# Kernel tuning notes

Measured on AMD Instinct MI355X. Metric: run time of the kernel, lower is better.

The kernel has to match this reference:

```python
import jax, jax.numpy as jnp
import numpy as np

B, T, F, H, L = 16384, 24, 7, 8, 4
DENSE = [T * H, 1024, 2048, 4]


def setup_inputs() -> dict:
    key = jax.random.key(0)
    d = {"x": jax.random.normal(jax.random.fold_in(key, 0), (B, T, F), jnp.float32)}
    k = 1
    s = 1.0 / np.sqrt(H)  # torch LSTM init bound
    for l in range(L):
        in_dim = F if l == 0 else H
        for name, shape in [("Wih", (4 * H, in_dim)), ("Whh", (4 * H, H)), ("bih", (4 * H,)), ("bhh", (4 * H,))]:
            d[f"{name}{l}"] = jax.random.uniform(jax.random.fold_in(key, k), shape, jnp.float32, -s, s)
            k += 1
    for i in range(1, len(DENSE)):
        si = 1.0 / np.sqrt(DENSE[i - 1])
        d[f"Wd{i}"] = jax.random.uniform(jax.random.fold_in(key, k), (DENSE[i], DENSE[i - 1]), jnp.float32, -si, si)
        k += 1
        d[f"bd{i}"] = jax.random.uniform(jax.random.fold_in(key, k), (DENSE[i],), jnp.float32, -si, si)
        k += 1
    return d


def _lstm_layer(xs, Wih, Whh, b):
    # xs: [T, B, in] -> ys: [T, B, H]; torch gate order i,f,g,o
    Hn = Whh.shape[1]
    h0 = jnp.zeros((xs.shape[1], Hn), xs.dtype)

    def step(carry, xt):
        h, c = carry
        z = xt @ Wih.T + h @ Whh.T + b  # [B, 4H]
        i, f, g, o = jnp.split(z, 4, axis=-1)
        c = jax.nn.sigmoid(f) * c + jax.nn.sigmoid(i) * jnp.tanh(g)
        h = jax.nn.sigmoid(o) * jnp.tanh(c)
        return (h, c), h

    (_, _), ys = jax.lax.scan(step, (h0, h0), xs)
    return ys


def _forward(x, lstm_params, dense_params):
    xs = jnp.transpose(x, (1, 0, 2))  # [T, B, F]
    for (Wih, Whh, bih, bhh) in lstm_params:
        xs = _lstm_layer(xs, Wih, Whh, bih + bhh)
    out = jnp.transpose(xs, (1, 0, 2)).reshape(x.shape[0], T * H)  # [B, 192]
    (W1, b1), (W2, b2), (W3, b3) = dense_params
    out = jax.nn.relu(out @ W1.T + b1)
    out = jax.nn.relu(out @ W2.T + b2)
    return out @ W3.T + b3  # [B, num_classes]


def reference(x, Wih0, Whh0, bih0, bhh0, Wih1, Whh1, bih1, bhh1, Wih2, Whh2, bih2, bhh2, Wih3, Whh3, bih3, bhh3, Wd1, bd1, Wd2, bd2, Wd3, bd3):
    lstm_params = [(Wih0, Whh0, bih0, bhh0), (Wih1, Whh1, bih1, bhh1), (Wih2, Whh2, bih2, bhh2), (Wih3, Whh3, bih3, bhh3)]
    dense_params = [(Wd1, bd1), (Wd2, bd2), (Wd3, bd3)]
    return _forward(x, lstm_params, dense_params)
```

## Files before the change

kernel.cpp:

```cpp
#include <hip/hip_runtime.h>
#include <hip/hip_bf16.h>

typedef __attribute__((ext_vector_type(4))) float f32x4;
typedef __attribute__((ext_vector_type(16))) float f32x16;
typedef __attribute__((ext_vector_type(2))) float f32x2;
typedef __attribute__((ext_vector_type(8))) short bf16x8;

__device__ __forceinline__ ushort f2bf(float f) {
    union { float f; uint u; } v; v.f = f;
    uint u = v.u;
    return (ushort)((u + 0x7fffu + ((u >> 16) & 1u)) >> 16);
}
__device__ __forceinline__ float sigm(float x) {
    return __builtin_amdgcn_rcpf(1.0f + __builtin_amdgcn_exp2f(x * -1.442695040888963f));
}
__device__ __forceinline__ float tanh_(float x) {
    return 2.0f * __builtin_amdgcn_rcpf(1.0f + __builtin_amdgcn_exp2f(x * -2.885390081777927f)) - 1.0f;
}

typedef const __attribute__((address_space(1))) unsigned int ga_u32;
typedef __attribute__((address_space(3))) unsigned int lds_u32;
__device__ __forceinline__ void g2l16(const void* g, void* l) {
    __builtin_amdgcn_global_load_lds((ga_u32*)(unsigned long long)g,
                                     (lds_u32*)(unsigned int)(unsigned long long)l,
                                     16, 0, 0);
}

struct LstmW {
    const float* wih[4];
    const float* whh[4];
    const float* bih[4];
    const float* bhh[4];
};

__device__ __forceinline__ void gates8p(const f32x2 w01[8], const f32x2 w23[8],
                                        const float xv8[8], f32x2& a01, f32x2& a23) {
#pragma unroll
    for (int k = 0; k < 8; ++k) {
        f32x2 xv = {xv8[k], xv8[k]};
        a01 += w01[k] * xv;
        a23 += w23[k] * xv;
    }
}
__device__ __forceinline__ void cellup(f32x2 a01, f32x2 a23, float& h, float& c) {
    c = sigm(a01.y) * c + sigm(a01.x) * tanh_(a23.x);
    h = sigm(a23.y) * tanh_(c);
}
__device__ __forceinline__ void ld8(const float* p, float v[8]) {
    float4 a = *(const float4*)p;
    float4 b = *(const float4*)(p + 4);
    v[0] = a.x; v[1] = a.y; v[2] = a.z; v[3] = a.w;
    v[4] = b.x; v[5] = b.y; v[6] = b.z; v[7] = b.w;
}

__global__ __launch_bounds__(256) void pre_kernel(const float* __restrict__ x, LstmW p,
                                                  ushort* __restrict__ Y,
                                                  const float* __restrict__ W1,
                                                  const float* __restrict__ W2,
                                                  ushort* __restrict__ W1b,
                                                  ushort* __restrict__ W2b,
                                                  const float* __restrict__ b3,
                                                  float* __restrict__ out) {
    __shared__ float xs[32 * 168];
    __shared__ float hb[32 * 200];

    const int tid = threadIdx.x;
    if (blockIdx.x >= 512) {
        const int tg = (blockIdx.x - 512) * 256 + tid;
        if (tg < 16384) {
            float4 bv = {b3[0], b3[1], b3[2], b3[3]};
            ((float4*)out)[tg] = bv;
        }
#pragma unroll
        for (int s = 0; s < 4; ++s) {
            int i = tg + s * 143360;
            const float4* src; ushort4* dst; int off;
            if (i < 49152) { src = (const float4*)W1; dst = (ushort4*)W1b; off = i; }
            else { src = (const float4*)W2; dst = (ushort4*)W2b; off = i - 49152; }
            float4 v = src[off];
            ushort4 r; r.x = f2bf(v.x); r.y = f2bf(v.y); r.z = f2bf(v.z); r.w = f2bf(v.w);
            dst[off] = r;
        }
        return;
    }

    const int e0 = blockIdx.x * 32;
    {
        const float4* s = (const float4*)(x + (size_t)e0 * 168);
        float4* d = (float4*)xs;
        for (int i = tid; i < 1344; i += 256) d[i] = s[i];
    }
    __syncthreads();

    const int el = tid >> 3, j = tid & 7;
    float* hr = hb + el * 200;
    const float* xr = xs + el * 168;

    f32x2 wx01[8], wx23[8], wh01[8], wh23[8], b01, b23;

    {
        const float* Wih = p.wih[0];
        const float* Whh = p.whh[0];
#pragma unroll
        for (int k = 0; k < 7; ++k) {
            wx01[k] = {Wih[(0 + j) * 7 + k], Wih[(8 + j) * 7 + k]};
            wx23[k] = {Wih[(16 + j) * 7 + k], Wih[(24 + j) * 7 + k]};
        }
#pragma unroll
        for (int k = 0; k < 8; ++k) {
            wh01[k] = {Whh[(0 + j) * 8 + k], Whh[(8 + j) * 8 + k]};
            wh23[k] = {Whh[(16 + j) * 8 + k], Whh[(24 + j) * 8 + k]};
        }
        b01 = {p.bih[0][j] + p.bhh[0][j], p.bih[0][8 + j] + p.bhh[0][8 + j]};
        b23 = {p.bih[0][16 + j] + p.bhh[0][16 + j], p.bih[0][24 + j] + p.bhh[0][24 + j]};

        float h = 0.f, c = 0.f;
        {
            f32x2 a01 = b01, a23 = b23;
#pragma unroll
            for (int k = 0; k < 7; ++k) {
                f32x2 xv = {xr[k], xr[k]};
                a01 += wx01[k] * xv; a23 += wx23[k] * xv;
            }
            cellup(a01, a23, h, c);
            hr[j] = h;
        }
        for (int t = 1; t < 24; ++t) {
            f32x2 a01 = b01, a23 = b23;
#pragma unroll
            for (int k = 0; k < 7; ++k) {
                f32x2 xv = {xr[t * 7 + k], xr[t * 7 + k]};
                a01 += wx01[k] * xv; a23 += wx23[k] * xv;
            }
            float hp[8]; ld8(&hr[(t - 1) * 8], hp);
            gates8p(wh01, wh23, hp, a01, a23);
            cellup(a01, a23, h, c);
            hr[t * 8 + j] = h;
        }
    }

#pragma unroll
    for (int l = 1; l < 4; ++l) {
        const float* Wih = p.wih[l];
        const float* Whh = p.whh[l];
#pragma unroll
        for (int k = 0; k < 8; ++k) {
            wx01[k] = {Wih[(0 + j) * 8 + k], Wih[(8 + j) * 8 + k]};
            wx23[k] = {Wih[(16 + j) * 8 + k], Wih[(24 + j) * 8 + k]};
            wh01[k] = {Whh[(0 + j) * 8 + k], Whh[(8 + j) * 8 + k]};
            wh23[k] = {Whh[(16 + j) * 8 + k], Whh[(24 + j) * 8 + k]};
        }
        b01 = {p.bih[l][j] + p.bhh[l][j], p.bih[l][8 + j] + p.bhh[l][8 + j]};
        b23 = {p.bih[l][16 + j] + p.bhh[l][16 + j], p.bih[l][24 + j] + p.bhh[l][24 + j]};

        float h = 0.f, c = 0.f;
        {
            float xin[8]; ld8(&hr[0], xin);
            f32x2 a01 = b01, a23 = b23;
            gates8p(wx01, wx23, xin, a01, a23);
            cellup(a01, a23, h, c);
            hr[j] = h;
            if (l == 3) Y[((size_t)(e0 + el) * 24) * 8 + j] = f2bf(h);
        }
        for (int t = 1; t < 24; ++t) {
            float xin[8]; ld8(&hr[t * 8], xin);
            float hp[8];  ld8(&hr[(t - 1) * 8], hp);
            f32x2 a01 = b01, a23 = b23;
            gates8p(wx01, wx23, xin, a01, a23);
            gates8p(wh01, wh23, hp, a01, a23);
            cellup(a01, a23, h, c);
            hr[t * 8 + j] = h;
            if (l == 3) Y[((size_t)(e0 + el) * 24 + t) * 8 + j] = f2bf(h);
        }
    }
}

template <int KDIM>
__device__ __forceinline__ void gemm_body(const ushort* __restrict__ A,
                                          const ushort* __restrict__ W,
                                          const float* __restrict__ bias,
                                          ushort* __restrict__ Hout, int N) {
    __shared__ alignas(16) ushort smem[16384];
    ushort* As = smem;
    ushort* Ws = smem + 8192;

    const int tid = threadIdx.x;
    const int m0 = blockIdx.x * 128;
    const int n0 = blockIdx.y * 128;
    const int lane = tid & 63;
    const int wv = tid >> 6;
    const int wm = (wv & 1) * 64;
    const int wn = (wv >> 1) * 64;
    const int l31 = lane & 31;
    const int kh = lane >> 5;

    const int lrow = lane >> 3;
    const int lchunk = (lane & 7) ^ lrow;
    const ushort* Ag = A + (size_t)(m0 + wv * 32 + lrow) * KDIM + lchunk * 8;
    const ushort* Wg = W + (size_t)(n0 + wv * 32 + lrow) * KDIM + lchunk * 8;
    ushort* Ald = As + wv * 2048;
    ushort* Wld = Ws + wv * 2048;

    const int r7 = l31 & 7;
    const int arow0 = (wm + l31) * 64;
    const int brow0 = (wn + l31) * 64;

    f32x16 acc[2][2];
#pragma unroll
    for (int mi = 0; mi < 2; ++mi)
#pragma unroll
        for (int ni = 0; ni < 2; ++ni)
#pragma unroll
            for (int r = 0; r < 16; ++r) acc[mi][ni][r] = 0.f;

    for (int k0 = 0; k0 < KDIM; k0 += 64) {
#pragma unroll
        for (int c = 0; c < 4; ++c)
            g2l16(Ag + (size_t)c * 8 * KDIM + k0, Ald + c * 512);
#pragma unroll
        for (int c = 0; c < 4; ++c)
            g2l16(Wg + (size_t)c * 8 * KDIM + k0, Wld + c * 512);
        __syncthreads();

#pragma unroll
        for (int ks = 0; ks < 4; ++ks) {
            const int ck = ((ks * 2 + kh) ^ r7) * 8;
            bf16x8 afr[2], bfr[2];
#pragma unroll
            for (int mi = 0; mi < 2; ++mi)
                afr[mi] = *(const bf16x8*)&As[arow0 + mi * 2048 + ck];
#pragma unroll
            for (int ni = 0; ni < 2; ++ni)
                bfr[ni] = *(const bf16x8*)&Ws[brow0 + ni * 2048 + ck];
#pragma unroll
            for (int mi = 0; mi < 2; ++mi)
#pragma unroll
                for (int ni = 0; ni < 2; ++ni)
                    acc[mi][ni] = __builtin_amdgcn_mfma_f32_32x32x16_bf16(afr[mi], bfr[ni],
                                                                         acc[mi][ni], 0, 0, 0);
        }
        __syncthreads();
    }

#pragma unroll
    for (int ni = 0; ni < 2; ++ni) {
        const int col = n0 + wn + ni * 32 + l31;
        const float b = bias[col];
#pragma unroll
        for (int mi = 0; mi < 2; ++mi)
#pragma unroll
            for (int r = 0; r < 16; ++r) {
                const int row = m0 + wm + mi * 32 + (r & 3) + 8 * (r >> 2) + 4 * kh;
                Hout[(size_t)row * N + col] = f2bf(fmaxf(acc[mi][ni][r] + b, 0.f));
            }
    }
}

__global__ __launch_bounds__(256, 4) void gemm1_kernel(const ushort* __restrict__ A,
                                                       const ushort* __restrict__ W,
                                                       const float* __restrict__ bias,
                                                       ushort* __restrict__ Hout, int N) {
    gemm_body<192>(A, W, bias, Hout, N);
}

template <int OFFB>
__device__ __forceinline__ bf16x8 dsr(unsigned a) {
    bf16x8 r;
    asm volatile("ds_read_b128 %0, %1 offset:%2"
                 : "=v"(r) : "v"(a), "i"(OFFB));
    return r;
}
template <int QA, int QB, int KS>
__device__ __forceinline__ void mma_sub(f32x4 acc[8][4], const bf16x8 afr[8],
                                        const bf16x8 br[4]) {
#pragma unroll
    for (int mi = 0; mi < 4; ++mi)
#pragma unroll
        for (int ni = 0; ni < 2; ++ni)
            acc[QA * 4 + mi][QB * 2 + ni] = __builtin_amdgcn_mfma_f32_16x16x32_bf16(
                afr[mi * 2 + KS], br[ni * 2 + KS], acc[QA * 4 + mi][QB * 2 + ni],
                0, 0, 0);
}

#define SBAR()  __builtin_amdgcn_s_barrier()
#define SCHED0() __builtin_amdgcn_sched_barrier(0)
#define LGKM(N) do { asm volatile("s_waitcnt lgkmcnt(" #N ")"); SCHED0(); } while (0)
#define VMC(N)  do { asm volatile("s_waitcnt vmcnt(" #N ")" ::: "memory"); } while (0)
#define PRIO1() __builtin_amdgcn_s_setprio(1)
#define PRIO0() do { __builtin_amdgcn_s_setprio(0); SCHED0(); } while (0)

__global__ __launch_bounds__(512) void gemm2_kernel(const ushort* __restrict__ A,
                                                    const ushort* __restrict__ W,
                                                    const float* __restrict__ bias,
                                                    const float* __restrict__ W3,
                                                    float* __restrict__ outf) {
    __shared__ alignas(16) ushort smem[65536];
    __shared__ alignas(16) float w3s[1040];

    const int tid = threadIdx.x;
    const int wg = ((int)blockIdx.x & 7) * 64 + ((int)blockIdx.x >> 3);
    const int m0 = (wg >> 3) << 8;
    const int n0 = (wg & 7) << 8;

    const int lane = tid & 63;
    const int wv = tid >> 6;

    const int lrow = tid >> 3;
    const int lc8 = ((tid & 7) ^ (lrow & 7)) << 3;
    const ushort* Ag = A + (size_t)(m0 + lrow) * 1024 + lc8;
    const ushort* Bg = W + (size_t)(n0 + lrow) * 1024 + lc8;
    ushort* const sA0 = smem;
    ushort* const sB0 = smem + 16384;
    ushort* const sA1 = smem + 32768;
    ushort* const sB1 = smem + 49152;
    const int srow64 = (wv << 3) * 64;

    const int l15 = lane & 15, kq = lane >> 4, r7 = l15 & 7;
    const int wM = wv >> 2, wN = wv & 3;
    const unsigned sbase = (unsigned)(unsigned long long)&smem[0];
    const unsigned pc0B = (unsigned)((kq ^ r7) << 4);
    const unsigned pc1B = pc0B ^ 64u;
    const unsigned aRowB = (unsigned)((wM * 128 + l15) * 128);
    const unsigned bRowB = (unsigned)((wN * 64 + l15) * 128);
    const unsigned aA0p0 = sbase + aRowB + pc0B;
    const unsigned aA0p1 = sbase + aRowB + pc1B;
    const unsigned aA1p0 = aA0p0 + 65536u;
    const unsigned aA1p1 = aA0p1 + 65536u;
    const unsigned bB0p0 = sbase + 32768u + bRowB + pc0B;
    const unsigned bB0p1 = sbase + 32768u + bRowB + pc1B;
    const unsigned bB1p0 = bB0p0 + 65536u;
    const unsigned bB1p1 = bB0p1 + 65536u;

    auto stA = [&](int buf, int h, int kt) {
        ushort* b = buf ? sA1 : sA0;
#pragma unroll
        for (int c = 0; c < 2; ++c)
            g2l16(Ag + (size_t)(h * 128 + c * 64) * 1024 + kt * 64,
                  b + (h * 128 + c * 64) * 64 + srow64);
    };
    auto stB = [&](int buf, int h, int kt) {
        ushort* b = buf ? sB1 : sB0;
#pragma unroll
        for (int c = 0; c < 2; ++c)
            g2l16(Bg + (size_t)(h * 128 + c * 64) * 1024 + kt * 64,
                  b + (h * 128 + c * 64) * 64 + srow64);
    };

    f32x4 acc[8][4];
#pragma unroll
    for (int i = 0; i < 8; ++i)
#pragma unroll
        for (int j = 0; j < 4; ++j)
#pragma unroll
            for (int r = 0; r < 4; ++r) acc[i][j][r] = 0.f;

#pragma unroll
    for (int i = 0; i < 2; ++i) {
        int idx = tid + i * 512;
        w3s[(idx >> 8) * 260 + (idx & 255)] = W3[(size_t)(idx >> 8) * 2048 + n0 + (idx & 255)];
    }
    float bias4[4];
#pragma unroll
    for (int ni = 0; ni < 4; ++ni) bias4[ni] = bias[n0 + wN * 64 + ni * 16 + l15];

    stA(0, 0, 0); stA(0, 1, 0); stB(0, 0, 0); stB(0, 1, 0);
    stB(1, 0, 1); stB(1, 1, 1);
    asm volatile("s_waitcnt lgkmcnt(0)");
    VMC(4);
    SBAR(); SCHED0();

    bf16x8 afr[8], b0r[4], b1r[4];
    afr[0] = dsr<0>(aA0p0);    afr[2] = dsr<2048>(aA0p0);
    afr[4] = dsr<4096>(aA0p0); afr[6] = dsr<6144>(aA0p0);
    b0r[0] = dsr<0>(bB0p0);    b0r[2] = dsr<2048>(bB0p0);

#pragma unroll 1
    for (int it = 0; it < 8; ++it) {
        const int k1 = 2 * it + 1, k2 = 2 * it + 2, k3 = 2 * it + 3;
        const bool nl = (it < 7);
        SBAR(); SCHED0();
        afr[1] = dsr<0>(aA0p1);    afr[3] = dsr<2048>(aA0p1);
        afr[5] = dsr<4096>(aA0p1); afr[7] = dsr<6144>(aA0p1);
        b0r[1] = dsr<0>(bB0p1);    b0r[3] = dsr<2048>(bB0p1);
        stA(1, 0, k1);
        LGKM(6); PRIO1(); mma_sub<0, 0, 0>(acc, afr, b0r); PRIO0();
        b1r[0] = dsr<4096>(bB0p0); b1r[2] = dsr<6144>(bB0p0);
        LGKM(2); PRIO1(); mma_sub<0, 0, 1>(acc, afr, b0r); PRIO0();
        SBAR(); SCHED0();
        b1r[1] = dsr<4096>(bB0p1); b1r[3] = dsr<6144>(bB0p1);
        stA(1, 1, k1);
        LGKM(2); PRIO1(); mma_sub<0, 1, 0>(acc, afr, b1r); PRIO0();
        afr[0] = dsr<8192>(aA0p0);  afr[2] = dsr<10240>(aA0p0);
        afr[4] = dsr<12288>(aA0p0); afr[6] = dsr<14336>(aA0p0);
        LGKM(4); PRIO1(); mma_sub<0, 1, 1>(acc, afr, b1r); PRIO0();
        SBAR(); SCHED0();
        afr[1] = dsr<8192>(aA0p1);  afr[3] = dsr<10240>(aA0p1);
        afr[5] = dsr<12288>(aA0p1); afr[7] = dsr<14336>(aA0p1);
        if (nl) stB(0, 0, k2);
        LGKM(4); PRIO1(); mma_sub<1, 1, 0>(acc, afr, b1r); PRIO0();
        LGKM(0); PRIO1(); mma_sub<1, 1, 1>(acc, afr, b1r); PRIO0();
        if (nl) { VMC(2); } else { VMC(0); }
        SBAR(); SCHED0();
        if (nl) stB(0, 1, k2);
        PRIO1(); mma_sub<1, 0, 0>(acc, afr, b0r); PRIO0();
        afr[0] = dsr<8192>(aA1p0);  afr[2] = dsr<10240>(aA1p0);
        afr[4] = dsr<12288>(aA1p0); afr[6] = dsr<14336>(aA1p0);
        b0r[0] = dsr<0>(bB1p0);     b0r[2] = dsr<2048>(bB1p0);
        PRIO1(); mma_sub<1, 0, 1>(acc, afr, b0r); PRIO0();
        SBAR(); SCHED0();
        afr[1] = dsr<8192>(aA1p1);  afr[3] = dsr<10240>(aA1p1);
        afr[5] = dsr<12288>(aA1p1); afr[7] = dsr<14336>(aA1p1);
        b0r[1] = dsr<0>(bB1p1);     b0r[3] = dsr<2048>(bB1p1);
        if (nl) stA(0, 0, k2);
        LGKM(6); PRIO1(); mma_sub<1, 0, 0>(acc, afr, b0r); PRIO0();
        b1r[0] = dsr<4096>(bB1p0); b1r[2] = dsr<6144>(bB1p0);
        LGKM(2); PRIO1(); mma_sub<1, 0, 1>(acc, afr, b0r); PRIO0();
        SBAR(); SCHED0();
        b1r[1] = dsr<4096>(bB1p1); b1r[3] = dsr<6144>(bB1p1);
        if (nl) stA(0, 1, k2);
        LGKM(2); PRIO1(); mma_sub<1, 1, 0>(acc, afr, b1r); PRIO0();
        afr[0] = dsr<0>(aA1p0);    afr[2] = dsr<2048>(aA1p0);
        afr[4] = dsr<4096>(aA1p0); afr[6] = dsr<6144>(aA1p0);
        LGKM(4); PRIO1(); mma_sub<1, 1, 1>(acc, afr, b1r); PRIO0();
        SBAR(); SCHED0();
        afr[1] = dsr<0>(aA1p1);    afr[3] = dsr<2048>(aA1p1);
        afr[5] = dsr<4096>(aA1p1); afr[7] = dsr<6144>(aA1p1);
        if (nl) stB(1, 0, k3);
        LGKM(4); PRIO1(); mma_sub<0, 1, 0>(acc, afr, b1r); PRIO0();
        LGKM(0); PRIO1(); mma_sub<0, 1, 1>(acc, afr, b1r); PRIO0();
        VMC(2);
        SBAR(); SCHED0();
        if (nl) stB(1, 1, k3);
        PRIO1(); mma_sub<0, 0, 0>(acc, afr, b0r); PRIO0();
        if (nl) {
            afr[0] = dsr<0>(aA0p0);    afr[2] = dsr<2048>(aA0p0);
            afr[4] = dsr<4096>(aA0p0); afr[6] = dsr<6144>(aA0p0);
            b0r[0] = dsr<0>(bB0p0);    b0r[2] = dsr<2048>(bB0p0);
        }
        PRIO1(); mma_sub<0, 0, 1>(acc, afr, b0r); PRIO0();
    }

    float* Cs = (float*)smem;
    const int drow = tid >> 3;
    const int cls = (tid & 7) >> 1;
    const int hf = tid & 1;
    const float* wrow = &w3s[cls * 260 + hf * 128];
    __syncthreads();
#pragma unroll
    for (int s = 0; s < 4; ++s) {
        if (wM == (s >> 1)) {
            const int mb = (s & 1) * 4;
#pragma unroll
            for (int mi = 0; mi < 4; ++mi)
#pragma unroll
                for (int ni = 0; ni < 4; ++ni) {
                    f32x4 v = acc[mb + mi][ni];
                    const int cbase = (mi * 16 + kq * 4) * 260 + wN * 64 + ni * 16 + l15;
#pragma unroll
                    for (int r = 0; r < 4; ++r)
                        Cs[cbase + r * 260] = fmaxf(v[r] + bias4[ni], 0.f);
                }
        }
        __syncthreads();
        {
            const float* crow = &Cs[drow * 260 + hf * 128];
            float p = 0.f;
#pragma unroll
            for (int ch = 0; ch < 64; ++ch) {
                f32x2 cv = *(const f32x2*)(crow + ch * 2);
                f32x2 wv2 = *(const f32x2*)(wrow + ch * 2);
                p += cv.x * wv2.x + cv.y * wv2.y;
            }
            p += __shfl_xor(p, 1);
            if (hf == 0)
                atomicAdd(&outf[(size_t)(m0 + s * 64 + drow) * 4 + cls], p);
        }
        __syncthreads();
    }
}

extern "C" void kernel_launch(void* const* d_in, const int* in_sizes, int n_in,
                              void* d_out, int out_size, void* d_ws, size_t ws_size,
                              hipStream_t stream) {
    const float* x = (const float*)d_in[0];
    LstmW w;
    for (int l = 0; l < 4; ++l) {
        w.wih[l] = (const float*)d_in[1 + 4 * l];
        w.whh[l] = (const float*)d_in[2 + 4 * l];
        w.bih[l] = (const float*)d_in[3 + 4 * l];
        w.bhh[l] = (const float*)d_in[4 + 4 * l];
    }
    const float* Wd1 = (const float*)d_in[17];
    const float* bd1 = (const float*)d_in[18];
    const float* Wd2 = (const float*)d_in[19];
    const float* bd2 = (const float*)d_in[20];
    const float* Wd3 = (const float*)d_in[21];
    const float* bd3 = (const float*)d_in[22];
    float* out = (float*)d_out;

    ushort* Y   = (ushort*)d_ws;
    ushort* H1  = (ushort*)((char*)d_ws + 6291456);
    ushort* W1b = (ushort*)((char*)d_ws + 39845888);
    ushort* W2b = (ushort*)((char*)d_ws + 40239104);

    pre_kernel<<<1072, 256, 0, stream>>>(x, w, Y, Wd1, Wd2, W1b, W2b, bd3, out);
    gemm1_kernel<<<dim3(128, 8), 256, 0, stream>>>(Y, W1b, bd1, H1, 1024);
    gemm2_kernel<<<512, 512, 0, stream>>>(H1, W2b, bd2, Wd3, out);
}
```

Measured before the change: 210.0 us.

## Issue A-tile prefetches earlier and restructure fused dense3 epilogue reduction

Moves each A-tile global-to-LDS prefetch one stage earlier in the GEMM main loop, adding one extra prefetch in the prologue and raising the vmcnt wait threshold to match, so loads overlap more MFMA work. It also rewrites the fused final-layer epilogue. Each thread now reads interleaved float4 chunks of the activation row and weights for all 4 classes, then does a 3-level shuffle reduction, replacing the previous 2-thread split per class. The earlier prefetch raises the risk of LDS hazards, and the new epilogue uses more shuffles.

```diff
diff --git a/kernel.cpp b/kernel.cpp
--- a/kernel.cpp
+++ b/kernel.cpp
@@ -364,9 +364,9 @@
     for (int ni = 0; ni < 4; ++ni) bias4[ni] = bias[n0 + wN * 64 + ni * 16 + l15];
 
     stA(0, 0, 0); stA(0, 1, 0); stB(0, 0, 0); stB(0, 1, 0);
-    stB(1, 0, 1); stB(1, 1, 1);
+    stB(1, 0, 1); stB(1, 1, 1); stA(1, 0, 1);
     asm volatile("s_waitcnt lgkmcnt(0)");
-    VMC(4);
+    VMC(6);
     SBAR(); SCHED0();
 
     bf16x8 afr[8], b0r[4], b1r[4];
@@ -382,13 +382,12 @@
         afr[1] = dsr<0>(aA0p1);    afr[3] = dsr<2048>(aA0p1);
         afr[5] = dsr<4096>(aA0p1); afr[7] = dsr<6144>(aA0p1);
         b0r[1] = dsr<0>(bB0p1);    b0r[3] = dsr<2048>(bB0p1);
-        stA(1, 0, k1);
+        stA(1, 1, k1);
         LGKM(6); PRIO1(); mma_sub<0, 0, 0>(acc, afr, b0r); PRIO0();
         b1r[0] = dsr<4096>(bB0p0); b1r[2] = dsr<6144>(bB0p0);
         LGKM(2); PRIO1(); mma_sub<0, 0, 1>(acc, afr, b0r); PRIO0();
         SBAR(); SCHED0();
         b1r[1] = dsr<4096>(bB0p1); b1r[3] = dsr<6144>(bB0p1);
-        stA(1, 1, k1);
         LGKM(2); PRIO1(); mma_sub<0, 1, 0>(acc, afr, b1r); PRIO0();
         afr[0] = dsr<8192>(aA0p0);  afr[2] = dsr<10240>(aA0p0);
         afr[4] = dsr<12288>(aA0p0); afr[6] = dsr<14336>(aA0p0);
@@ -401,7 +400,7 @@
         LGKM(0); PRIO1(); mma_sub<1, 1, 1>(acc, afr, b1r); PRIO0();
         if (nl) { VMC(2); } else { VMC(0); }
         SBAR(); SCHED0();
-        if (nl) stB(0, 1, k2);
+        if (nl) { stB(0, 1, k2); stA(0, 0, k2); }
         PRIO1(); mma_sub<1, 0, 0>(acc, afr, b0r); PRIO0();
         afr[0] = dsr<8192>(aA1p0);  afr[2] = dsr<10240>(aA1p0);
         afr[4] = dsr<12288>(aA1p0); afr[6] = dsr<14336>(aA1p0);
@@ -411,13 +410,12 @@
         afr[1] = dsr<8192>(aA1p1);  afr[3] = dsr<10240>(aA1p1);
         afr[5] = dsr<12288>(aA1p1); afr[7] = dsr<14336>(aA1p1);
         b0r[1] = dsr<0>(bB1p1);     b0r[3] = dsr<2048>(bB1p1);
-        if (nl) stA(0, 0, k2);
+        if (nl) stA(0, 1, k2);
         LGKM(6); PRIO1(); mma_sub<1, 0, 0>(acc, afr, b0r); PRIO0();
         b1r[0] = dsr<4096>(bB1p0); b1r[2] = dsr<6144>(bB1p0);
         LGKM(2); PRIO1(); mma_sub<1, 0, 1>(acc, afr, b0r); PRIO0();
         SBAR(); SCHED0();
         b1r[1] = dsr<4096>(bB1p1); b1r[3] = dsr<6144>(bB1p1);
-        if (nl) stA(0, 1, k2);
         LGKM(2); PRIO1(); mma_sub<1, 1, 0>(acc, afr, b1r); PRIO0();
         afr[0] = dsr<0>(aA1p0);    afr[2] = dsr<2048>(aA1p0);
         afr[4] = dsr<4096>(aA1p0); afr[6] = dsr<6144>(aA1p0);
@@ -428,9 +426,9 @@
         if (nl) stB(1, 0, k3);
         LGKM(4); PRIO1(); mma_sub<0, 1, 0>(acc, afr, b1r); PRIO0();
         LGKM(0); PRIO1(); mma_sub<0, 1, 1>(acc, afr, b1r); PRIO0();
-        VMC(2);
-        SBAR(); SCHED0();
-        if (nl) stB(1, 1, k3);
+        if (nl) { VMC(2); }
+        SBAR(); SCHED0();
+        if (nl) { stB(1, 1, k3); stA(1, 0, k3); }
         PRIO1(); mma_sub<0, 0, 0>(acc, afr, b0r); PRIO0();
         if (nl) {
             afr[0] = dsr<0>(aA0p0);    afr[2] = dsr<2048>(aA0p0);
@@ -442,9 +440,7 @@
 
     float* Cs = (float*)smem;
     const int drow = tid >> 3;
-    const int cls = (tid & 7) >> 1;
-    const int hf = tid & 1;
-    const float* wrow = &w3s[cls * 260 + hf * 128];
+    const int j8 = tid & 7;
     __syncthreads();
 #pragma unroll
     for (int s = 0; s < 4; ++s) {
@@ -463,17 +459,26 @@
         }
         __syncthreads();
         {
-            const float* crow = &Cs[drow * 260 + hf * 128];
-            float p = 0.f;
-#pragma unroll
-            for (int ch = 0; ch < 64; ++ch) {
-                f32x2 cv = *(const f32x2*)(crow + ch * 2);
-                f32x2 wv2 = *(const f32x2*)(wrow + ch * 2);
-                p += cv.x * wv2.x + cv.y * wv2.y;
+            const float* crow = &Cs[drow * 260 + j8 * 4];
+            f32x4 pp = {0.f, 0.f, 0.f, 0.f};
+#pragma unroll
+            for (int k = 0; k < 8; ++k) {
+                f32x4 cv = *(const f32x4*)(crow + k * 32);
+#pragma unroll
+                for (int q = 0; q < 4; ++q) {
+                    f32x4 wv4 = *(const f32x4*)(&w3s[q * 260 + j8 * 4 + k * 32]);
+                    pp[q] += cv[0] * wv4[0] + cv[1] * wv4[1] + cv[2] * wv4[2] + cv[3] * wv4[3];
+                }
             }
-            p += __shfl_xor(p, 1);
-            if (hf == 0)
-                atomicAdd(&outf[(size_t)(m0 + s * 64 + drow) * 4 + cls], p);
+#pragma unroll
+            for (int m = 1; m < 8; m <<= 1) {
+#pragma unroll
+                for (int q = 0; q < 4; ++q) pp[q] += __shfl_xor(pp[q], m);
+            }
+            const float pv = (j8 == 0) ? pp[0] : (j8 == 1) ? pp[1]
+                           : (j8 == 2) ? pp[2] : pp[3];
+            if (j8 < 4)
+                atomicAdd(&outf[(size_t)(m0 + s * 64 + drow) * 4 + j8], pv);
         }
         __syncthreads();
     }
```

Measured after the change: 211.3 us, median of 2. About the same (+0.6%).
